# Performance work log

Measured on AMD Instinct MI355X. Metric: run time of the kernel, lower is better.

The kernel has to match this reference:

```python
import jax, jax.numpy as jnp
import numpy as np

N = 64
DX = np.pi / N
# torch.fft.fftfreq(N+1, d) == np.fft.fftfreq(N+1) / d ; d varies per env so keep base freqs
BASE_FREQ = (2.0 * np.pi * np.fft.fftfreq(N + 1)).astype(np.float32)  # [65]
DOMAIN = np.array([0.75, 1.0, 0.75, 1.0, 0.75, 1.0, 0.75, 1.0], dtype=np.float32)


def _poisson_solve(w, dx_b):
    # w: [B,N,N] vorticity (already negated), dx_b: [B]
    w_pad = jnp.pad(w, ((0, 0), (0, 1), (0, 1)), mode='wrap')          # circular pad (0,1,0,1) -> [B,65,65]
    wf = jnp.fft.fft2(w_pad / (N ** 2))
    f = BASE_FREQ[None, :] / dx_b[:, None]                             # [B,65] per-env wavenumbers
    k2 = f[:, :, None] ** 2 + f[:, None, :] ** 2                       # [B,65,65] (meshgrid 'ij': kxx^2+kyy^2)
    uf = -wf / (1e-12 + k2)
    uf = uf.at[:, 0, 0].set(0.0)
    return jnp.fft.ifft2((N ** 2) * uf).real[:, :N, :N]                # [B,N,N]


def reference(t, y0, env, params):
    x = y0[:, 0]                                                       # [B,N,N]
    env = env.astype(jnp.int32)
    mu = params[env, 0][:, None, None]                                 # [B,1,1]
    fdx = (jnp.asarray(DOMAIN)[env] * DX)[:, None, None]               # [B,1,1]

    psi = _poisson_solve(-x, fdx[:, 0, 0])

    dxp = lambda a: jnp.roll(a, -1, axis=2) - jnp.roll(a, 1, axis=2)   # derive_x
    dyp = lambda a: jnp.roll(a, -1, axis=1) - jnp.roll(a, 1, axis=1)   # derive_y
    inv4 = 1.0 / (4.0 * fdx ** 2)

    J1 = (dyp(psi) * dxp(x) - dxp(psi) * dyp(x)) * inv4
    J2 = (jnp.roll(x, -1, axis=2) * dyp(jnp.roll(psi, -1, axis=2))
          - jnp.roll(x, 1, axis=2) * dyp(jnp.roll(psi, 1, axis=2))
          - jnp.roll(x, -1, axis=1) * dxp(jnp.roll(psi, -1, axis=1))
          + jnp.roll(x, 1, axis=1) * dxp(jnp.roll(psi, 1, axis=1))) * inv4
    J3 = (jnp.roll(x, (-1, -1), axis=(1, 2)) * (jnp.roll(psi, -1, axis=1) - jnp.roll(psi, -1, axis=2))
          - jnp.roll(x, (1, 1), axis=(1, 2)) * (jnp.roll(psi, 1, axis=2) - jnp.roll(psi, 1, axis=1))
          - jnp.roll(x, (-1, 1), axis=(1, 2)) * (jnp.roll(psi, -1, axis=1) - jnp.roll(psi, 1, axis=2))
          + jnp.roll(x, (1, -1), axis=(1, 2)) * (jnp.roll(psi, -1, axis=2) - jnp.roll(psi, 1, axis=1))) * inv4

    # circular-pad conv2d with kernel [[0,1,0],[1,-4,1],[1,1,0]] == cross-correlation stencil below
    lap = (jnp.roll(x, 1, axis=1) + jnp.roll(x, -1, axis=1)
           + jnp.roll(x, 1, axis=2) + jnp.roll(x, -1, axis=2)
           + jnp.roll(x, (-1, 1), axis=(1, 2)) - 4.0 * x) / (fdx ** 2)

    dudt = -(J1 + J2 + J3) / 3.0 + mu * lap
    return dudt[:, None]                                               # [B,1,N,N]


def setup_inputs() -> dict:
    key = jax.random.key(0)
    k1, k2 = jax.random.split(key)
    B, n_env = 2048, 8
    y0 = jax.random.normal(k1, (B, 1, N, N), dtype=jnp.float32)
    env = jax.random.randint(k2, (B,), 0, n_env, dtype=jnp.int64)
    params = jnp.concatenate([jnp.full((n_env, 1), 0.005, jnp.float32),
                              jnp.full((n_env, 1), 1.0, jnp.float32)], axis=1)
    t = jnp.zeros((1,), dtype=jnp.float32)
    return {"t": t, "y0": y0, "env": env, "params": params}
```

## Files before the change

kernel.cpp:

```cpp
#include <hip/hip_runtime.h>
#include <math.h>

#define P65 65
#define PLANE_U16 5248
#define SIDE_OFF  5120
#define PSI_U16   8320

__device__ __align__(16) ushort gAfrag[18*512];
__device__ float  g_MpN[65*65];
__device__ float  g64tab[64];

__device__ __constant__ float c_DOMAIN[8] = {0.75f,1.0f,0.75f,1.0f,0.75f,1.0f,0.75f,1.0f};

__device__ inline ushort f2bf(float f) {
  unsigned u = __float_as_uint(f);
  return (ushort)((u + 0x7FFFu + ((u >> 16) & 1u)) >> 16);
}
__device__ inline float bf2f(ushort h) { return __uint_as_float(((unsigned)h) << 16); }

__device__ inline double Gval(int r, int i) {
  int m = (r <= 32) ? r : (r - 32);
  int prod = (m * (i % 65)) % 65;
  double ang = 6.283185307179586476925286766559 * (double)prod / 65.0;
  return (r <= 32) ? cos(ang) : sin(ang);
}
__device__ inline double Gfold(int r, int i) {
  double v = Gval(r, i);
  if (i == 0) v += Gval(r, 64);
  return v;
}

__global__ void init_tables() {
  int tid = blockIdx.x*blockDim.x + threadIdx.x;
  int nth = gridDim.x*blockDim.x;
  for (int idx = tid; idx < 18*512; idx += nth) {
    int blk = idx >> 9, rem = idx & 511;
    int lane = rem >> 3, e = rem & 7;
    int i16 = lane & 15, kg = lane >> 4;
    float v = 0.f;
    if (blk < 10) {
      int mt = blk >> 1, kt = blk & 1;
      int r = 16*mt + i16;
      int i = 32*kt + 8*kg + e;
      if (r < 65 && i < 64) v = (float)Gfold(r, i);
    } else {
      int b2 = blk - 10;
      int mt = b2 >> 1, kt = b2 & 1;
      int j  = 16*mt + i16;
      int k1 = 32*kt + 8*kg + e;
      if (j < 64 && k1 < 64) v = (float)Gval(k1, j);
    }
    gAfrag[idx] = f2bf(v);
  }
  for (int idx = tid; idx < 65*65; idx += nth) {
    int k1 = idx/65, k2 = idx%65;
    float v = 0.f;
    if (k1 | k2) {
      double n1 = (k1==0)?(1.0/65.0):(2.0/65.0);
      double n2 = (k2==0)?(1.0/65.0):(2.0/65.0);
      int m1 = (k1<=32)?k1:(k1-32), m2 = (k2<=32)?k2:(k2-32);
      double b1 = 6.283185307179586476925286766559*(double)m1/65.0;
      double b2 = 6.283185307179586476925286766559*(double)m2/65.0;
      v = (float)((n1*n2)/(b1*b1 + b2*b2));
    }
    g_MpN[idx] = v;
  }
  for (int idx = tid; idx < 64; idx += nth)
    g64tab[idx] = (float)Gval(64, idx);
}

typedef __attribute__((ext_vector_type(8))) short bf16x8;
typedef __attribute__((ext_vector_type(4))) float f32x4;

template<int MT, int NT, int MR, int NR, int TBLOFF, bool SCALE, bool RK, bool PSI>
__device__ inline void stage(const ushort* __restrict__ Lin,
                             ushort* __restrict__ Lout,
                             float* __restrict__ psiout,
                             int wvu, int lane)
{
  const int lg = lane >> 4, li = lane & 15;
  for (int tile = wvu; tile < MT*NT; tile += 8) {
    int mt = tile / NT, nt = tile - mt*NT;
    int n = 16*nt + li;
    f32x4 acc = {0.f, 0.f, 0.f, 0.f};
    #pragma unroll
    for (int kt = 0; kt < 2; ++kt) {
      bf16x8 af = *(const bf16x8*)(gAfrag + (TBLOFF + mt*2 + kt)*512 + lane*8);
      bf16x8 bfr = *(const bf16x8*)(Lin + (nt*2 + kt)*512 + lane*8);
      acc = __builtin_amdgcn_mfma_f32_16x16x32_bf16(af, bfr, acc, 0, 0, 0);
    }
    float rkB = 0.f;
    if (RK) rkB = bf2f(Lin[SIDE_OFF + n]);
    int mbase = 16*mt + 4*lg;
    int wbase = (mt*2 + (nt>>1))*512 + ((2*nt + (li>>3))&3)*128 + (li&7);
    #pragma unroll
    for (int r = 0; r < 4; ++r) {
      int m = mbase + r;
      if (m < MR && n < NR) {
        float v = acc[r];
        if (SCALE) v *= g_MpN[m*65 + n];
        if (RK)    v = fmaf(g64tab[m], rkB, v);
        if (PSI) {
          psiout[n*P65 + m] = v;
        } else if (NT == 5 && nt == 4) {
          Lout[SIDE_OFF + m] = f2bf(v);
        } else {
          Lout[wbase + (4*lg + r)*8] = f2bf(v);
        }
      }
    }
  }
}

__device__ inline float shflx(float v, int srclane) { return __shfl(v, srclane, 64); }

__global__ void __launch_bounds__(512) pde_main(const float* __restrict__ y0,
                                                const int*   __restrict__ env,
                                                const float* __restrict__ params,
                                                float*       __restrict__ out)
{
  __shared__ __align__(16) ushort Lsh[PLANE_U16 + PSI_U16];
  ushort* PB   = Lsh;
  ushort* PA   = Lsh + PLANE_U16;
  float*  Ppsi = (float*)(Lsh + PLANE_U16);

  const int b    = blockIdx.x;
  const int t    = threadIdx.x;
  const int lane = t & 63;
  const int wvu  = __builtin_amdgcn_readfirstlane(t >> 6);

  const int   e       = env[b];
  const float mu      = params[2*e];
  const float fdx     = c_DOMAIN[e] * (float)(3.14159265358979323846/64.0);
  const float inv_dx2 = 1.0f/(fdx*fdx);

  const float* xb = y0 + (size_t)b*4096;

  float xr[8];
  bf16x8 hv;
  #pragma unroll
  for (int k=0;k<8;++k) {
    float v = xb[(8*wvu + k)*64 + lane];
    xr[k] = v;
    hv[k] = (short)f2bf(v);
  }
  {
    int wb = ((lane>>4)*2 + (wvu>>2))*512 + ((wvu&3)*16 + (lane&15))*8;
    *(bf16x8*)(PA + wb) = hv;
  }
  __syncthreads();

  stage<5,4,65,64, 0,false,false,false>(PA, PB, nullptr, wvu, lane);
  __syncthreads();
  stage<5,5,65,65, 0,true ,false,false>(PB, PA, nullptr, wvu, lane);
  __syncthreads();
  stage<4,5,64,65,10,false,true ,false>(PA, PB, nullptr, wvu, lane);
  __syncthreads();
  stage<4,4,64,64,10,false,true ,true >(PB, nullptr, Ppsi, wvu, lane);
  __syncthreads();

  {
    const int c = lane, cm = (c+63)&63, cp = (c+1)&63;
    const int j0 = wvu*8, jm0 = (j0+63)&63, jp8 = (j0+8)&63;
    float xbm = xb[jm0*64 + c];
    float xbp = xb[jp8*64 + c];
    float* op = out + (size_t)b*4096;

    float xm_c = xbm,   xm_m = shflx(xm_c, cm), xm_p = shflx(xm_c, cp);
    float xc_c = xr[0], xc_m = shflx(xc_c, cm), xc_p = shflx(xc_c, cp);
    float pm_m = Ppsi[jm0*P65+cm], pm_c = Ppsi[jm0*P65+c], pm_p = Ppsi[jm0*P65+cp];
    float pc_m = Ppsi[j0 *P65+cm], pc_c = Ppsi[j0 *P65+c], pc_p = Ppsi[j0 *P65+cp];

    #pragma unroll
    for (int m=0;m<8;++m) {
      int j = j0 + m, jp = (j+1)&63;
      float xn_c = (m < 7) ? xr[m+1] : xbp;
      float xn_m = shflx(xn_c, cm), xn_p = shflx(xn_c, cp);
      float pn_m = Ppsi[jp*P65+cm], pn_c = Ppsi[jp*P65+c], pn_p = Ppsi[jp*P65+cp];

      float J1 = (pn_c - pm_c)*(xc_p - xc_m) - (pc_p - pc_m)*(xn_c - xm_c);
      float J2 = xc_p*(pn_p - pm_p) - xc_m*(pn_m - pm_m)
               - xn_c*(pn_p - pn_m) + xm_c*(pm_p - pm_m);
      float J3 = xn_p*(pn_c - pc_p) - xm_m*(pc_m - pm_c)
               - xn_m*(pn_c - pc_m) + xm_p*(pc_p - pm_c);
      float lap = (xm_c + xn_c + xc_m + xc_p + xn_m - 4.0f*xc_c) * inv_dx2;

      op[j*64 + c] = -(J1 + J2 + J3)*(0.25f/3.0f) + mu*lap;

      xm_m=xc_m; xm_c=xc_c; xm_p=xc_p;  pm_m=pc_m; pm_c=pc_c; pm_p=pc_p;
      xc_m=xn_m; xc_c=xn_c; xc_p=xn_p;  pc_m=pn_m; pc_c=pn_c; pc_p=pn_p;
    }
  }
}

extern "C" void kernel_launch(void* const* d_in, const int* in_sizes, int n_in,
                              void* d_out, int out_size, void* d_ws, size_t ws_size,
                              hipStream_t stream) {
  const float* y0     = (const float*)d_in[1];
  const int*   env    = (const int*)  d_in[2];
  const float* params = (const float*)d_in[3];
  float*       out    = (float*)d_out;
  int B = in_sizes[1] / 4096;

  init_tables<<<32, 256, 0, stream>>>();
  pde_main<<<B, 512, 0, stream>>>(y0, env, params, out);
}
```

Measured before the change: 41.52 us.

## Use float trig in table init and unroll per-wave MFMA tile loop

The table-initialization kernel now computes its DFT basis and Poisson scaling tables in single precision instead of double, and launches twice as many blocks. This is meant to cut the cost of the slow double-precision cos/sin in the init kernel, at some loss of table accuracy before bf16 rounding. The per-wave tile loop in each MFMA stage is also fully unrolled with a fixed trip count and a predicated store, so the compiler can interleave independent tile loads and MFMAs.

```diff
diff --git a/kernel.cpp b/kernel.cpp
--- a/kernel.cpp
+++ b/kernel.cpp
@@ -18,15 +18,15 @@
 }
 __device__ inline float bf2f(ushort h) { return __uint_as_float(((unsigned)h) << 16); }
 
-__device__ inline double Gval(int r, int i) {
+__device__ inline float Gvalf(int r, int i) {
   int m = (r <= 32) ? r : (r - 32);
   int prod = (m * (i % 65)) % 65;
-  double ang = 6.283185307179586476925286766559 * (double)prod / 65.0;
-  return (r <= 32) ? cos(ang) : sin(ang);
-}
-__device__ inline double Gfold(int r, int i) {
-  double v = Gval(r, i);
-  if (i == 0) v += Gval(r, 64);
+  float ang = 6.2831853071795864769f * (float)prod / 65.0f;
+  return (r <= 32) ? cosf(ang) : sinf(ang);
+}
+__device__ inline float Gfoldf(int r, int i) {
+  float v = Gvalf(r, i);
+  if (i == 0) v += Gvalf(r, 64);
   return v;
 }
 
@@ -42,13 +42,13 @@
       int mt = blk >> 1, kt = blk & 1;
       int r = 16*mt + i16;
       int i = 32*kt + 8*kg + e;
-      if (r < 65 && i < 64) v = (float)Gfold(r, i);
+      if (r < 65 && i < 64) v = Gfoldf(r, i);
     } else {
       int b2 = blk - 10;
       int mt = b2 >> 1, kt = b2 & 1;
       int j  = 16*mt + i16;
       int k1 = 32*kt + 8*kg + e;
-      if (j < 64 && k1 < 64) v = (float)Gval(k1, j);
+      if (j < 64 && k1 < 64) v = Gvalf(k1, j);
     }
     gAfrag[idx] = f2bf(v);
   }
@@ -56,17 +56,17 @@
     int k1 = idx/65, k2 = idx%65;
     float v = 0.f;
     if (k1 | k2) {
-      double n1 = (k1==0)?(1.0/65.0):(2.0/65.0);
-      double n2 = (k2==0)?(1.0/65.0):(2.0/65.0);
+      float n1 = (k1==0)?(1.0f/65.0f):(2.0f/65.0f);
+      float n2 = (k2==0)?(1.0f/65.0f):(2.0f/65.0f);
       int m1 = (k1<=32)?k1:(k1-32), m2 = (k2<=32)?k2:(k2-32);
-      double b1 = 6.283185307179586476925286766559*(double)m1/65.0;
-      double b2 = 6.283185307179586476925286766559*(double)m2/65.0;
-      v = (float)((n1*n2)/(b1*b1 + b2*b2));
+      float b1 = 6.2831853071795864769f*(float)m1/65.0f;
+      float b2 = 6.2831853071795864769f*(float)m2/65.0f;
+      v = (n1*n2)/(b1*b1 + b2*b2);
     }
     g_MpN[idx] = v;
   }
   for (int idx = tid; idx < 64; idx += nth)
-    g64tab[idx] = (float)Gval(64, idx);
+    g64tab[idx] = Gvalf(64, idx);
 }
 
 typedef __attribute__((ext_vector_type(8))) short bf16x8;
@@ -79,8 +79,14 @@
                              int wvu, int lane)
 {
   const int lg = lane >> 4, li = lane & 15;
-  for (int tile = wvu; tile < MT*NT; tile += 8) {
-    int mt = tile / NT, nt = tile - mt*NT;
+  constexpr int NTL = MT*NT;
+  constexpr int TPW = (NTL + 7) >> 3;
+  #pragma unroll
+  for (int tb = 0; tb < TPW; ++tb) {
+    int tile = wvu + 8*tb;
+    bool act = (tile < NTL);
+    int tl = act ? tile : 0;
+    int mt = tl / NT, nt = tl - mt*NT;
     int n = 16*nt + li;
     f32x4 acc = {0.f, 0.f, 0.f, 0.f};
     #pragma unroll
@@ -96,7 +102,7 @@
     #pragma unroll
     for (int r = 0; r < 4; ++r) {
       int m = mbase + r;
-      if (m < MR && n < NR) {
+      if (act && m < MR && n < NR) {
         float v = acc[r];
         if (SCALE) v *= g_MpN[m*65 + n];
         if (RK)    v = fmaf(g64tab[m], rkB, v);
@@ -202,6 +208,6 @@
   float*       out    = (float*)d_out;
   int B = in_sizes[1] / 4096;
 
-  init_tables<<<32, 256, 0, stream>>>();
+  init_tables<<<64, 256, 0, stream>>>();
   pde_main<<<B, 512, 0, stream>>>(y0, env, params, out);
 }
```

Result: no change. 41.53 us (+0.0%).
